# Optimization experiments

Hardware: AMD Instinct MI355X
Metric: run time of the kernel (lower is better)

Reference implementation:

```python
import jax, jax.numpy as jnp
import numpy as np

B, N, C_IN = 16, 1024, 768
H, KQ, VD = 8, 256, 512          # num_heads, kq_dim, v_dim per head
NH_V = H * VD                    # 4096
D_OUT = 512
SCALE = D_OUT ** -0.5            # module uses dim_out**-0.5
EPS = 1e-5


def _bn(x, gamma, beta, mean, var):
    # eval-mode BatchNorm1d over last dim
    return (x - mean) * (gamma * jax.lax.rsqrt(var + EPS)) + beta


def setup_inputs() -> dict:
    key = jax.random.key(0)
    ks = jax.random.split(key, 8)
    return {
        "x": jax.random.normal(ks[0], (B, N, C_IN), jnp.float32),
        "qkv_w": jax.random.normal(ks[1], (2 * H * KQ + NH_V, C_IN), jnp.float32) * 0.02,
        "qkv_gamma": jax.random.uniform(ks[2], (2 * H * KQ + NH_V,), jnp.float32),
        "qkv_beta": jax.random.normal(ks[3], (2 * H * KQ + NH_V,), jnp.float32) * 0.02,
        "qkv_mean": jax.random.normal(ks[4], (2 * H * KQ + NH_V,), jnp.float32) * 0.02,
        "qkv_var": jnp.ones((2 * H * KQ + NH_V,), jnp.float32),
        "pos_bias": jax.random.normal(ks[5], (H, N, N), jnp.float32),
        "proj_w": jax.random.normal(ks[6], (D_OUT, NH_V), jnp.float32) * 0.02,
        "proj_gamma": jax.random.uniform(ks[7], (D_OUT,), jnp.float32),
        "proj_beta": jnp.zeros((D_OUT,), jnp.float32),
        "proj_mean": jnp.zeros((D_OUT,), jnp.float32),
        "proj_var": jnp.ones((D_OUT,), jnp.float32),
    }


def reference(x, qkv_w, qkv_gamma, qkv_beta, qkv_mean, qkv_var,
              pos_bias, proj_w, proj_gamma, proj_beta, proj_mean, proj_var):
    b, n, _ = x.shape
    qkv = _bn(x @ qkv_w.T, qkv_gamma, qkv_beta, qkv_mean, qkv_var)  # [B,N,h]
    qkv = qkv.reshape(b, n, H, 2 * KQ + VD)
    q, k, v = jnp.split(qkv, [KQ, 2 * KQ], axis=3)                  # [B,N,H,*]
    attn = jnp.einsum('bnhd,bmhd->bhnm', q, k) * SCALE + pos_bias   # [B,H,N,N]
    attn = jax.nn.softmax(attn, axis=-1)
    out = jnp.einsum('bhnm,bmhd->bnhd', attn, v).reshape(b, n, NH_V)
    out = jnp.clip(out, -1.0, 1.0)                                  # Hardtanh
    return _bn(out @ proj_w.T, proj_gamma, proj_beta, proj_mean, proj_var)
```

## Files before the change

kernel.cpp:

```cpp
#include <hip/hip_runtime.h>

using v8bf  = __bf16 __attribute__((ext_vector_type(8)));
using v16f  = float  __attribute__((ext_vector_type(16)));

#define EPS_BN 1e-5f
#define ATT_SCALE 0.044194173824159216f

__device__ __forceinline__ unsigned short f2bf(float f){
  union { float f; unsigned int u; } c; c.f = f;
  unsigned int u = c.u + 0x7fffu + ((c.u >> 16) & 1u);
  return (unsigned short)(u >> 16);
}

__device__ __forceinline__ v8bf ld8(const unsigned short* p){
  union { uint4 u; v8bf v; } c;
  c.u = *(const uint4*)p;
  return c.v;
}

__device__ __forceinline__ void glds16(const unsigned short* g, unsigned short* l){
  __builtin_amdgcn_global_load_lds(
      (const __attribute__((address_space(1))) void*)g,
      (__attribute__((address_space(3))) void*)l, 16, 0, 0);
}

__global__ void cast_bf16_kernel(const float* __restrict__ src,
                                 unsigned short* __restrict__ dst, int n8){
  int i = blockIdx.x * 256 + threadIdx.x;
  if (i >= n8) return;
  const float4* s4 = (const float4*)src;
  float4 a = s4[2*i], b = s4[2*i+1];
  union { unsigned short s[8]; uint4 u; } r;
  r.s[0]=f2bf(a.x); r.s[1]=f2bf(a.y); r.s[2]=f2bf(a.z); r.s[3]=f2bf(a.w);
  r.s[4]=f2bf(b.x); r.s[5]=f2bf(b.y); r.s[6]=f2bf(b.z); r.s[7]=f2bf(b.w);
  ((uint4*)dst)[i] = r.u;
}

__global__ void bn_precompute(const float* __restrict__ g, const float* __restrict__ be,
                              const float* __restrict__ mn, const float* __restrict__ vr,
                              float* __restrict__ scale, float* __restrict__ shift,
                              int n, int qfold){
  int i = blockIdx.x * 256 + threadIdx.x;
  if (i >= n) return;
  float s = g[i] * rsqrtf(vr[i] + EPS_BN);
  float t = be[i] - mn[i] * s;
  if (qfold && (i & 1023) < 256){ s *= ATT_SCALE; t *= ATT_SCALE; }
  scale[i] = s; shift[i] = t;
}

template<int MODE>
__launch_bounds__(256, 2)
__global__ void gemm_nt(const unsigned short* __restrict__ A,
                        const unsigned short* __restrict__ Bm,
                        int K, long sA, long sB, long mbase,
                        const float* __restrict__ scale, const float* __restrict__ shift,
                        const float* __restrict__ sums,
                        unsigned short* __restrict__ ob16,
                        float* __restrict__ outf)
{
  __shared__ __align__(16) unsigned short As[8192];
  __shared__ __align__(16) unsigned short Bs[8192];
  const int tid = threadIdx.x;
  const int w = tid >> 6, lane = tid & 63, ln = lane & 31, lg = lane >> 5;
  const int wm = (w >> 1) * 64, wn = (w & 1) * 64;
  const long bm = (long)blockIdx.y * 128, bn = (long)blockIdx.x * 128;
  const int z = blockIdx.z;
  const unsigned short* Ab = A + (MODE == 3 ? 0L : (long)z * sA) + bm * K;
  const unsigned short* Bb = Bm + (MODE == 3 ? 0L : (long)z * sB) + bn * K;

  const int kbeg = (MODE == 3) ? z * (K >> 2) : 0;
  const int kend = (MODE == 3) ? kbeg + (K >> 2) : K;

  const int rsub = lane >> 3;
  const int gsl  = lane & 7;
  const unsigned short* gA[4]; const unsigned short* gB[4];
  unsigned short *lA[4], *lB[4];
  #pragma unroll
  for (int i = 0; i < 4; i++){
    int r = w*32 + i*8 + rsub;
    int go = (gsl ^ (r & 7)) * 8;
    gA[i] = Ab + (long)r * K + go;
    gB[i] = Bb + (long)r * K + go;
    lA[i] = As + (w*32 + i*8) * 64;
    lB[i] = Bs + (w*32 + i*8) * 64;
  }

  v16f acc[2][2];
  #pragma unroll
  for (int a = 0; a < 2; a++)
    #pragma unroll
    for (int b = 0; b < 2; b++)
      #pragma unroll
      for (int i = 0; i < 16; i++) acc[a][b][i] = 0.f;

  for (int k0 = kbeg; k0 < kend; k0 += 64){
    __syncthreads();
    #pragma unroll
    for (int i = 0; i < 4; i++){
      glds16(gA[i] + k0, lA[i]);
      glds16(gB[i] + k0, lB[i]);
    }
    __syncthreads();
    #pragma unroll
    for (int kk = 0; kk < 4; kk++){
      v8bf af[2], bfr[2];
      #pragma unroll
      for (int t = 0; t < 2; t++){
        int Ra = wm + t*32 + ln;
        af[t] = *(const v8bf*)&As[Ra*64 + ((kk*2 + lg) ^ (Ra & 7))*8];
        int Rb = wn + t*32 + ln;
        bfr[t] = *(const v8bf*)&Bs[Rb*64 + ((kk*2 + lg) ^ (Rb & 7))*8];
      }
      #pragma unroll
      for (int tm = 0; tm < 2; tm++)
        #pragma unroll
        for (int tn = 0; tn < 2; tn++)
          acc[tm][tn] = __builtin_amdgcn_mfma_f32_32x32x16_bf16(af[tm], bfr[tn], acc[tm][tn], 0, 0, 0);
    }
  }

  float invs[2][16];
  if (MODE == 1){
    #pragma unroll
    for (int tm = 0; tm < 2; tm++)
      #pragma unroll
      for (int i = 0; i < 16; i++){
        long gm = bm + wm + tm*32 + (i&3) + 8*(i>>2) + 4*lg;
        invs[tm][i] = 1.0f / sums[(long)z*1024 + gm];
      }
  }

  #pragma unroll
  for (int tm = 0; tm < 2; tm++){
    #pragma unroll
    for (int tn = 0; tn < 2; tn++){
      long gn = bn + wn + tn*32 + ln;
      float sc = 0.f, sh = 0.f;
      if (MODE == 0){ sc = scale[gn]; sh = shift[gn]; }
      #pragma unroll
      for (int i = 0; i < 16; i++){
        long gm = bm + wm + tm*32 + (i&3) + 8*(i>>2) + 4*lg;
        float v = acc[tm][tn][i];
        if (MODE == 0){
          ob16[gm*8192 + gn] = f2bf(v * sc + sh);
        } else if (MODE == 1){
          v = v * invs[tm][i];
          v = fminf(1.f, fmaxf(-1.f, v));
          int b2 = z >> 3, hh = z & 7;
          ob16[((long)b2*1024 + gm)*4096 + hh*512 + gn] = f2bf(v);
        } else {
          outf[((long)z * mbase + gm)*512 + gn] = v;
        }
      }
    }
  }
}

__global__ void reduce_bn(const float* __restrict__ part,
                          const float* __restrict__ sc, const float* __restrict__ sh,
                          float* __restrict__ out, long Mtot, long mbase){
  long idx = (long)blockIdx.x * 256 + threadIdx.x;
  if (idx >= Mtot * 128) return;
  long gm = idx >> 7;
  int gn4 = (int)(idx & 127) * 4;
  long PS = Mtot * 512;
  const float* p = part + gm*512 + gn4;
  float4 p0 = *(const float4*)(p);
  float4 p1 = *(const float4*)(p + PS);
  float4 p2 = *(const float4*)(p + 2*PS);
  float4 p3 = *(const float4*)(p + 3*PS);
  float4 s4 = *(const float4*)(sc + gn4);
  float4 h4 = *(const float4*)(sh + gn4);
  float4 r;
  r.x = (p0.x+p1.x+p2.x+p3.x)*s4.x + h4.x;
  r.y = (p0.y+p1.y+p2.y+p3.y)*s4.y + h4.y;
  r.z = (p0.z+p1.z+p2.z+p3.z)*s4.z + h4.z;
  r.w = (p0.w+p1.w+p2.w+p3.w)*s4.w + h4.w;
  *(float4*)(out + (mbase + gm)*512 + gn4) = r;
}

__global__ void transpose_v(const unsigned short* __restrict__ qkv,
                            unsigned short* __restrict__ Vt){
  __shared__ __align__(16) unsigned short Ts[64*72];
  const int bh = blockIdx.z;
  const int b2 = bh >> 3, h = bh & 7;
  const int n0 = blockIdx.x * 64, d0 = blockIdx.y * 64;
  const int tid = threadIdx.x;
  const unsigned short* Vb = qkv + (long)b2*1024*8192 + h*1024 + 512;
  unsigned short* Vtb = Vt + (long)bh * 524288;
  #pragma unroll
  for (int i = 0; i < 2; i++){
    int seg = tid + i*256;
    int row = seg >> 3, co = (seg & 7) * 8;
    *(uint4*)&Ts[row*72 + co] = *(const uint4*)(Vb + (long)(n0 + row)*8192 + d0 + co);
  }
  __syncthreads();
  #pragma unroll
  for (int i = 0; i < 2; i++){
    int seg = tid + i*256;
    int drow = seg >> 3, nco = (seg & 7) * 8;
    union { unsigned short s[8]; uint4 u; } r;
    #pragma unroll
    for (int j = 0; j < 8; j++) r.s[j] = Ts[(nco + j)*72 + drow];
    *(uint4*)(Vtb + (long)(d0 + drow)*1024 + n0 + nco) = r.u;
  }
}

__launch_bounds__(128, 2)
__global__ void attn_scores(const unsigned short* __restrict__ qkv,
                            const float* __restrict__ bias,
                            unsigned short* __restrict__ E,
                            float* __restrict__ sums)
{
  __shared__ __align__(16) unsigned short Ks[2][32*256];
  const int bh = blockIdx.y, mblk = blockIdx.x;
  const int b2 = bh >> 3, h = bh & 7;
  const int tid = threadIdx.x, w = tid >> 6, lane = tid & 63, ln = lane & 31, lg = lane >> 5;
  const int m0 = mblk * 64 + w * 32;
  const unsigned short* qbase = qkv + (long)b2*1024*8192 + h*1024;
  const unsigned short* kbase = qbase + 256;
  const float* biash = bias + (long)h * 1048576;
  unsigned short* Eb = E + (long)bh * 1048576;

  v8bf qf[16];
  {
    const unsigned short* qrow = qbase + (long)(m0 + ln)*8192 + lg*8;
    #pragma unroll
    for (int kf = 0; kf < 16; kf++) qf[kf] = ld8(qrow + kf*16);
  }

  const int rr = lane >> 5, slot = lane & 31;

  float sm[16];
  #pragma unroll
  for (int i = 0; i < 16; i++) sm[i] = 0.f;

  #pragma unroll
  for (int i = 0; i < 8; i++){
    int row = w*16 + i*2 + rr;
    glds16(kbase + (long)row*8192 + (slot ^ row)*8, &Ks[0][(w*16 + i*2)*256]);
  }

  for (int t = 0; t < 32; t++){
    __syncthreads();
    const int cb = t & 1;
    if (t < 31){
      const int nb = cb ^ 1;
      #pragma unroll
      for (int i = 0; i < 8; i++){
        int row = w*16 + i*2 + rr;
        glds16(kbase + (long)((t+1)*32 + row)*8192 + (slot ^ row)*8,
               &Ks[nb][(w*16 + i*2)*256]);
      }
    }
    v16f a0, a1;
    #pragma unroll
    for (int i = 0; i < 16; i++){ a0[i] = 0.f; a1[i] = 0.f; }
    #pragma unroll
    for (int kf = 0; kf < 16; kf += 2){
      v8bf k0 = *(const v8bf*)&Ks[cb][ln*256 + ((2*kf   + lg) ^ ln)*8];
      v8bf k1 = *(const v8bf*)&Ks[cb][ln*256 + ((2*kf+2 + lg) ^ ln)*8];
      a0 = __builtin_amdgcn_mfma_f32_32x32x16_bf16(qf[kf],   k0, a0, 0, 0, 0);
      a1 = __builtin_amdgcn_mfma_f32_32x32x16_bf16(qf[kf+1], k1, a1, 0, 0, 0);
    }
    const int col = t*32 + ln;
    #pragma unroll
    for (int q = 0; q < 4; q++){
      #pragma unroll
      for (int j = 0; j < 4; j++){
        int i = q*4 + j;
        int r = 4*lg + 8*q + j;
        float e = __expf(a0[i] + a1[i] + biash[(long)(m0 + r)*1024 + col]);
        sm[i] += e;
        Eb[(long)(m0 + r)*1024 + col] = f2bf(e);
      }
    }
  }

  #pragma unroll
  for (int i = 0; i < 16; i++){
    #pragma unroll
    for (int d = 1; d < 32; d <<= 1) sm[i] += __shfl_xor(sm[i], d, 64);
  }
  if (ln == 0){
    float* sp = sums + (long)bh * 1024 + m0 + 4*lg;
    #pragma unroll
    for (int q = 0; q < 4; q++)
      #pragma unroll
      for (int j = 0; j < 4; j++)
        sp[8*q + j] = sm[q*4 + j];
  }
}

extern "C" void kernel_launch(void* const* d_in, const int* in_sizes, int n_in,
                              void* d_out, int out_size, void* d_ws, size_t ws_size,
                              hipStream_t stream)
{
  const float* x        = (const float*)d_in[0];
  const float* qkv_w    = (const float*)d_in[1];
  const float* qg       = (const float*)d_in[2];
  const float* qb       = (const float*)d_in[3];
  const float* qm       = (const float*)d_in[4];
  const float* qv       = (const float*)d_in[5];
  const float* pos_bias = (const float*)d_in[6];
  const float* pw       = (const float*)d_in[7];
  const float* pg       = (const float*)d_in[8];
  const float* pbt      = (const float*)d_in[9];
  const float* pmn      = (const float*)d_in[10];
  const float* pvr      = (const float*)d_in[11];
  float* out = (float*)d_out;

  const unsigned long FIXED = 16846848UL;
  const unsigned long PERG  = 43548672UL;
  long G = 1;
  if      (ws_size >= FIXED + PERG*16) G = 16;
  else if (ws_size >= FIXED + PERG*8)  G = 8;
  else if (ws_size >= FIXED + PERG*4)  G = 4;
  else if (ws_size >= FIXED + PERG*2)  G = 2;
  else if (ws_size >= FIXED + PERG)    G = 1;
  else return;

  char* ws = (char*)d_ws;
  unsigned short* wqb = (unsigned short*)(ws + 0L);
  unsigned short* wpb = (unsigned short*)(ws + 12582912L);
  float* sc_qkv       = (float*)(ws + 16777216L);
  float* sh_qkv       = (float*)(ws + 16809984L);
  float* sc_p         = (float*)(ws + 16842752L);
  float* sh_p         = (float*)(ws + 16844800L);
  const long gb = 16846848L;
  unsigned short* xbg   = (unsigned short*)(ws + gb);
  unsigned short* qkvg  = (unsigned short*)(ws + gb + G*1572864L);
  unsigned short* Vtg   = (unsigned short*)(ws + gb + G*18350080L);
  unsigned short* Eg    = (unsigned short*)(ws + gb + G*26738688L);
  float* sumsg          = (float*)(ws + gb + G*43515904L);
  unsigned short* outcg = qkvg;
  float* partials       = (float*)Eg;

  cast_bf16_kernel<<<dim3(3072), 256, 0, stream>>>(qkv_w, wqb, 786432);
  cast_bf16_kernel<<<dim3(1024), 256, 0, stream>>>(pw,    wpb, 262144);
  bn_precompute<<<dim3(32), 256, 0, stream>>>(qg, qb, qm, qv, sc_qkv, sh_qkv, 8192, 1);
  bn_precompute<<<dim3(2),  256, 0, stream>>>(pg, pbt, pmn, pvr, sc_p, sh_p, 512, 0);

  const int nG = (int)(16 / G);
  for (int g = 0; g < nG; g++){
    const float* xg = x + (long)g * G * 786432L;
    long mbase = (long)g * G * 1024L;

    cast_bf16_kernel<<<dim3((unsigned)(G*384)), 256, 0, stream>>>(xg, xbg, (int)(G*98304));

    gemm_nt<0><<<dim3(64, (unsigned)(8*G), 1), 256, 0, stream>>>(
        xbg, wqb, 768, 0L, 0L, 0L, sc_qkv, sh_qkv, nullptr, qkvg, nullptr);

    transpose_v<<<dim3(16, 8, (unsigned)(8*G)), 256, 0, stream>>>(qkvg, Vtg);

    attn_scores<<<dim3(16, (unsigned)(8*G)), 128, 0, stream>>>(qkvg, pos_bias, Eg, sumsg);

    gemm_nt<1><<<dim3(4, 8, (unsigned)(8*G)), 256, 0, stream>>>(
        Eg, Vtg, 1024, 1048576L, 524288L, 0L, nullptr, nullptr, sumsg, outcg, nullptr);

    gemm_nt<3><<<dim3(4, (unsigned)(8*G), 4), 256, 0, stream>>>(
        outcg, wpb, 4096, 0L, 0L, (long)(G*1024), nullptr, nullptr, nullptr,
        nullptr, partials);

    reduce_bn<<<dim3((unsigned)(G*512)), 256, 0, stream>>>(
        partials, sc_p, sh_p, out, (long)(G*1024), mbase);
  }
}
```

Before: 1.053 ms.

## Split attention score computation across key blocks with partial row sums

Adds a grid z-dimension so each attn_scores block handles a quarter of the key columns, writing partial softmax denominators that the PV GEMM sums before normalising. It also prefetches the positional bias into registers before the MFMA loop and spreads the QK accumulation over four independent accumulators to shorten dependency chains. The aim is more blocks in flight to hide latency on a launch that previously had only 16x8G blocks. The partial sums reuse the x-cast buffer as scratch, which is safe only because xbg is dead by the time attn_scores runs.

```diff
diff --git a/kernel.cpp b/kernel.cpp
--- a/kernel.cpp
+++ b/kernel.cpp
@@ -5,6 +5,7 @@
 
 #define EPS_BN 1e-5f
 #define ATT_SCALE 0.044194173824159216f
+#define KSPLIT 4
 
 __device__ __forceinline__ unsigned short f2bf(float f){
   union { float f; unsigned int u; } c; c.f = f;
@@ -126,7 +127,9 @@
       #pragma unroll
       for (int i = 0; i < 16; i++){
         long gm = bm + wm + tm*32 + (i&3) + 8*(i>>2) + 4*lg;
-        invs[tm][i] = 1.0f / sums[(long)z*1024 + gm];
+        const float* sp = sums + (long)z * (KSPLIT*1024L) + gm;
+        float s = sp[0] + sp[1024] + sp[2048] + sp[3072];
+        invs[tm][i] = 1.0f / s;
       }
   }
 
@@ -210,10 +213,10 @@
 __global__ void attn_scores(const unsigned short* __restrict__ qkv,
                             const float* __restrict__ bias,
                             unsigned short* __restrict__ E,
-                            float* __restrict__ sums)
+                            float* __restrict__ psums)
 {
   __shared__ __align__(16) unsigned short Ks[2][32*256];
-  const int bh = blockIdx.y, mblk = blockIdx.x;
+  const int bh = blockIdx.y, mblk = blockIdx.x, zz = blockIdx.z;
   const int b2 = bh >> 3, h = bh & 7;
   const int tid = threadIdx.x, w = tid >> 6, lane = tid & 63, ln = lane & 31, lg = lane >> 5;
   const int m0 = mblk * 64 + w * 32;
@@ -235,16 +238,20 @@
   #pragma unroll
   for (int i = 0; i < 16; i++) sm[i] = 0.f;
 
+  const int NT = 32 / KSPLIT;
+  const int t0 = zz * NT;
+
   #pragma unroll
   for (int i = 0; i < 8; i++){
     int row = w*16 + i*2 + rr;
-    glds16(kbase + (long)row*8192 + (slot ^ row)*8, &Ks[0][(w*16 + i*2)*256]);
-  }
-
-  for (int t = 0; t < 32; t++){
+    glds16(kbase + (long)(t0*32 + row)*8192 + (slot ^ row)*8, &Ks[0][(w*16 + i*2)*256]);
+  }
+
+  for (int tt = 0; tt < NT; tt++){
+    const int t = t0 + tt;
     __syncthreads();
-    const int cb = t & 1;
-    if (t < 31){
+    const int cb = tt & 1;
+    if (tt < NT - 1){
       const int nb = cb ^ 1;
       #pragma unroll
       for (int i = 0; i < 8; i++){
@@ -253,24 +260,33 @@
                &Ks[nb][(w*16 + i*2)*256]);
       }
     }
-    v16f a0, a1;
-    #pragma unroll
-    for (int i = 0; i < 16; i++){ a0[i] = 0.f; a1[i] = 0.f; }
-    #pragma unroll
-    for (int kf = 0; kf < 16; kf += 2){
-      v8bf k0 = *(const v8bf*)&Ks[cb][ln*256 + ((2*kf   + lg) ^ ln)*8];
-      v8bf k1 = *(const v8bf*)&Ks[cb][ln*256 + ((2*kf+2 + lg) ^ ln)*8];
-      a0 = __builtin_amdgcn_mfma_f32_32x32x16_bf16(qf[kf],   k0, a0, 0, 0, 0);
-      a1 = __builtin_amdgcn_mfma_f32_32x32x16_bf16(qf[kf+1], k1, a1, 0, 0, 0);
-    }
+
     const int col = t*32 + ln;
+    float br[16];
+    #pragma unroll
+    for (int q = 0; q < 4; q++)
+      #pragma unroll
+      for (int j = 0; j < 4; j++)
+        br[q*4 + j] = biash[(long)(m0 + 4*lg + 8*q + j)*1024 + col];
+
+    v16f a[4];
+    #pragma unroll
+    for (int c = 0; c < 4; c++)
+      #pragma unroll
+      for (int i = 0; i < 16; i++) a[c][i] = 0.f;
+    #pragma unroll
+    for (int kb = 0; kb < 16; kb++){
+      v8bf kf8 = *(const v8bf*)&Ks[cb][ln*256 + ((2*kb + lg) ^ ln)*8];
+      a[kb & 3] = __builtin_amdgcn_mfma_f32_32x32x16_bf16(qf[kb], kf8, a[kb & 3], 0, 0, 0);
+    }
+
     #pragma unroll
     for (int q = 0; q < 4; q++){
       #pragma unroll
       for (int j = 0; j < 4; j++){
         int i = q*4 + j;
         int r = 4*lg + 8*q + j;
-        float e = __expf(a0[i] + a1[i] + biash[(long)(m0 + r)*1024 + col]);
+        float e = __expf((a[0][i] + a[1][i]) + (a[2][i] + a[3][i]) + br[i]);
         sm[i] += e;
         Eb[(long)(m0 + r)*1024 + col] = f2bf(e);
       }
@@ -283,7 +299,7 @@
     for (int d = 1; d < 32; d <<= 1) sm[i] += __shfl_xor(sm[i], d, 64);
   }
   if (ln == 0){
-    float* sp = sums + (long)bh * 1024 + m0 + 4*lg;
+    float* sp = psums + ((long)bh * KSPLIT + zz)*1024 + m0 + 4*lg;
     #pragma unroll
     for (int q = 0; q < 4; q++)
       #pragma unroll
@@ -335,6 +351,8 @@
   float* sumsg          = (float*)(ws + gb + G*43515904L);
   unsigned short* outcg = qkvg;
   float* partials       = (float*)Eg;
+  float* psums          = (float*)xbg;
+  (void)sumsg;
 
   cast_bf16_kernel<<<dim3(3072), 256, 0, stream>>>(qkv_w, wqb, 786432);
   cast_bf16_kernel<<<dim3(1024), 256, 0, stream>>>(pw,    wpb, 262144);
@@ -353,10 +371,11 @@
 
     transpose_v<<<dim3(16, 8, (unsigned)(8*G)), 256, 0, stream>>>(qkvg, Vtg);
 
-    attn_scores<<<dim3(16, (unsigned)(8*G)), 128, 0, stream>>>(qkvg, pos_bias, Eg, sumsg);
+    attn_scores<<<dim3(16, (unsigned)(8*G), KSPLIT), 128, 0, stream>>>(
+        qkvg, pos_bias, Eg, psums);
 
     gemm_nt<1><<<dim3(4, 8, (unsigned)(8*G)), 256, 0, stream>>>(
-        Eg, Vtg, 1024, 1048576L, 524288L, 0L, nullptr, nullptr, sumsg, outcg, nullptr);
+        Eg, Vtg, 1024, 1048576L, 524288L, 0L, nullptr, nullptr, psums, outcg, nullptr);
 
     gemm_nt<3><<<dim3(4, (unsigned)(8*G), 4), 256, 0, stream>>>(
         outcg, wpb, 4096, 0L, 0L, (long)(G*1024), nullptr, nullptr, nullptr,
```

New measurement: 1.153 ms. +9.4%, slower.
